# Performance work log

Measured on AMD Instinct MI355X. Metric: run time of the kernel, lower is better.

## Reference

```python
import jax, jax.numpy as jnp
import numpy as np
import itertools

# The repo's eset_ops_4_to_4 builds 69 permutation-equivariant basis ops on a
# rank-4 set tensor x[n, d, i, j, k, l]. We reconstruct the 69-dim basis as all
# order-preserving subset matchings (A, B) with A = kept input index slots,
# B = output slots receiving them (|A| = |B| = s, s = 1..4): sum x over the
# complement of A, then broadcast the reduced tensor into output positions B.
# Count: sum_{s=1..4} C(4,s)^2 = 16 + 36 + 16 + 1 = 69 (Vandermonde C(8,4)=70
# minus the s=0 global-sum term).

def _basis_pairs():
    pairs = []
    for s in range(1, 5):
        for A in itertools.combinations(range(4), s):
            for B in itertools.combinations(range(4), s):
                pairs.append((A, B))
    return pairs  # len == 69

_PAIRS = _basis_pairs()


def _forward(x, coefs, bias):
    # x: (n, d, N, N, N, N); coefs: (d, s_out, 69); bias: (1, s_out, 1,1,1,1)
    out_shape = (x.shape[0], coefs.shape[1]) + x.shape[2:]
    out = jnp.zeros(out_shape, x.dtype)
    for idx, (A, B) in enumerate(_PAIRS):
        sum_axes = tuple(2 + i for i in range(4) if i not in A)
        red = x.sum(axis=sum_axes) if sum_axes else x  # (n, d, N^|A|)
        # mix channels on the SMALL reduced tensor (op and channel mix commute)
        term = jnp.einsum('ds,nd...->ns...', coefs[:, :, idx], red)
        # place kept axes at output slots B (order-preserving), broadcast rest
        for p in range(4):
            if p not in B:
                term = jnp.expand_dims(term, axis=2 + p)
        out = out + term  # broadcasting add == broadcast then accumulate
    return out + bias


def setup_inputs() -> dict:
    key = jax.random.key(0)
    k1, k2 = jax.random.split(key)
    n, d, s_out, N, basis = 2, 8, 8, 32, 69
    x = jax.random.normal(k1, (n, d, N, N, N, N), dtype=jnp.float32)
    std = np.sqrt(2.0 / (d + s_out + basis)).astype(np.float32)
    coefs = std * jax.random.normal(k2, (d, s_out, basis), dtype=jnp.float32)
    bias = jnp.zeros((1, s_out, 1, 1, 1, 1), dtype=jnp.float32)
    return {'x': x, 'coefs': coefs, 'bias': bias}


def reference(x, coefs, bias):
    return _forward(x, coefs, bias)
```

## Files before the change

kernel.cpp:

```cpp
#include <hip/hip_runtime.h>


constexpr size_t R3SZ  = 524288;
constexpr size_t R2SZ  = 16384;
constexpr size_t R1SZ  = 512;
constexpr size_t R3OFF = 0;
constexpr size_t R2OFF = R3OFF + 4 * R3SZ;
constexpr size_t R1OFF = R2OFF + 6 * R2SZ;
constexpr size_t T2OFF = R1OFF + 4 * R1SZ;
constexpr size_t T1OFF = T2OFF + 6 * R2SZ;
constexpr size_t U3OFF = T1OFF + 4 * R1SZ;

__global__ __launch_bounds__(512) void k_red3(const float* __restrict__ x,
                                              float* __restrict__ ws) {
    __shared__ float4 cp[32][4][8];
    __shared__ float  b012[1024];
    __shared__ float4 a2[256];
    const int bid  = blockIdx.x;
    const int t    = threadIdx.x;
    const int half = t >> 8;
    const int tt   = t & 255;
    const int k    = tt >> 3;
    const int l4   = tt & 7;

    if (bid < 512) {
        const int i    = bid & 31;
        const int nd   = bid >> 5;
        const int w4   = (t >> 6) & 3;
        const int lane = t & 63;
        const float* xp = x + ((size_t)nd << 20) + ((size_t)i << 15) + k * 32 + l4 * 4;
        float4 acc = {0.f, 0.f, 0.f, 0.f};
        #pragma unroll
        for (int it = 0; it < 16; ++it) {
            const int j = it * 2 + half;
            float4 v = *(const float4*)(xp + j * 1024);
            acc.x += v.x; acc.y += v.y; acc.z += v.z; acc.w += v.w;
            float h = v.x + v.y + v.z + v.w;
            h += __shfl_xor(h, 1); h += __shfl_xor(h, 2); h += __shfl_xor(h, 4);
            if (l4 == 0) b012[j * 32 + k] = h;
            v.x += __shfl_xor(v.x, 8);  v.y += __shfl_xor(v.y, 8);
            v.z += __shfl_xor(v.z, 8);  v.w += __shfl_xor(v.w, 8);
            v.x += __shfl_xor(v.x, 16); v.y += __shfl_xor(v.y, 16);
            v.z += __shfl_xor(v.z, 16); v.w += __shfl_xor(v.w, 16);
            v.x += __shfl_xor(v.x, 32); v.y += __shfl_xor(v.y, 32);
            v.z += __shfl_xor(v.z, 32); v.w += __shfl_xor(v.w, 32);
            if (lane < 8) cp[j][w4][lane] = v;
        }
        if (half == 1) a2[tt] = acc;
        __syncthreads();
        const size_t base = ((size_t)nd << 15) + ((size_t)i << 10);
        *(float2*)(ws + R3OFF + base + 2 * t) = *(const float2*)(b012 + 2 * t);
        if (half == 0) {
            const int j = tt >> 3, lj = tt & 7;
            float4 s0 = cp[j][0][lj], s1 = cp[j][1][lj];
            float4 s2 = cp[j][2][lj], s3 = cp[j][3][lj];
            float4 s;
            s.x = s0.x + s1.x + s2.x + s3.x;
            s.y = s0.y + s1.y + s2.y + s3.y;
            s.z = s0.z + s1.z + s2.z + s3.z;
            s.w = s0.w + s1.w + s2.w + s3.w;
            *(float4*)(ws + R3OFF + R3SZ + base + j * 32 + lj * 4) = s;
            float4 b = a2[tt];
            a2[tt] = s;
            acc.x += b.x; acc.y += b.y; acc.z += b.z; acc.w += b.w;
            *(float4*)(ws + R3OFF + 2 * R3SZ + base + k * 32 + l4 * 4) = acc;
        }
        __syncthreads();
        const size_t r2b = (size_t)nd * 1024 + (size_t)i * 32;
        if (t < 32) {
            float s = 0.f;
            #pragma unroll
            for (int kk = 0; kk < 32; ++kk) s += b012[t * 32 + ((kk + t) & 31)];
            ws[R2OFF + 0 * R2SZ + r2b + t] = s;
        } else if (t < 64) {
            const int kc = t - 32;
            float s = 0.f;
            #pragma unroll
            for (int j = 0; j < 32; ++j) s += b012[j * 32 + kc];
            ws[R2OFF + 1 * R2SZ + r2b + kc] = s;
        } else if (t < 96) {
            const int l = t - 64;
            const float* af = (const float*)a2;
            float s = 0.f;
            #pragma unroll
            for (int j = 0; j < 32; ++j) s += af[j * 32 + l];
            ws[R2OFF + 2 * R2SZ + r2b + l] = s;
        }
    } else {
        const int bb = bid - 512;
        const int j  = bb & 31;
        const int nd = bb >> 5;
        const float* xp = x + ((size_t)nd << 20) + (size_t)j * 1024 + (size_t)tt * 4;
        float4 acc = {0.f, 0.f, 0.f, 0.f};
        #pragma unroll
        for (int it = 0; it < 16; ++it) {
            const int i = it * 2 + half;
            float4 v = *(const float4*)(xp + ((size_t)i << 15));
            acc.x += v.x; acc.y += v.y; acc.z += v.z; acc.w += v.w;
        }
        if (half == 1) a2[tt] = acc;
        __syncthreads();
        const size_t r2b = (size_t)nd * 1024 + (size_t)j * 32;
        if (half == 0) {
            float4 b = a2[tt];
            acc.x += b.x; acc.y += b.y; acc.z += b.z; acc.w += b.w;
            *(float4*)(ws + R3OFF + 3 * R3SZ + ((size_t)nd << 15)
                       + ((size_t)j << 10) + tt * 4) = acc;
            float h = acc.x + acc.y + acc.z + acc.w;
            h += __shfl_xor(h, 1); h += __shfl_xor(h, 2); h += __shfl_xor(h, 4);
            if ((t & 7) == 0) ws[R2OFF + 3 * R2SZ + r2b + k] = h;
            float4 c2 = acc;
            c2.x += __shfl_xor(c2.x, 8);  c2.y += __shfl_xor(c2.y, 8);
            c2.z += __shfl_xor(c2.z, 8);  c2.w += __shfl_xor(c2.w, 8);
            c2.x += __shfl_xor(c2.x, 16); c2.y += __shfl_xor(c2.y, 16);
            c2.z += __shfl_xor(c2.z, 16); c2.w += __shfl_xor(c2.w, 16);
            c2.x += __shfl_xor(c2.x, 32); c2.y += __shfl_xor(c2.y, 32);
            c2.z += __shfl_xor(c2.z, 32); c2.w += __shfl_xor(c2.w, 32);
            if ((t & 63) < 8) cp[0][t >> 6][t & 63] = c2;
        }
        __syncthreads();
        if (t < 8) {
            float4 s0 = cp[0][0][t], s1 = cp[0][1][t];
            float4 s2 = cp[0][2][t], s3 = cp[0][3][t];
            float4 s;
            s.x = s0.x + s1.x + s2.x + s3.x;
            s.y = s0.y + s1.y + s2.y + s3.y;
            s.z = s0.z + s1.z + s2.z + s3.z;
            s.w = s0.w + s1.w + s2.w + s3.w;
            *(float4*)(ws + R2OFF + 4 * R2SZ + r2b + t * 4) = s;
        }
    }
}

__global__ __launch_bounds__(256) void k_mixT(const float* __restrict__ coefs,
                                              float* __restrict__ ws) {
    __shared__ float cs[4416];
    __shared__ float s23[256];
    __shared__ float r1[1024];
    const int tt = threadIdx.x;
    for (int idx = tt; idx < 4416; idx += 256) cs[idx] = coefs[idx];
    const int b = blockIdx.x;
    if (b < 64) {
        const int n  = b >> 5;
        const int ch = b & 31;
        {
            const int d  = tt >> 5, q0 = tt & 31;
            const float* r023p = ws + R3OFF + 2 * R3SZ
                                 + ((size_t)(n * 8 + d) << 15) + ch * 32 + q0;
            float s = 0.f;
            #pragma unroll
            for (int i = 0; i < 32; ++i) s += r023p[i * 1024];
            s23[d * 32 + q0] = s;
        }
        __syncthreads();
        const int so = tt >> 5, pql = tt & 31;
        const int pq = ch * 32 + pql;
        float r2v[5][8];
        #pragma unroll
        for (int a2 = 0; a2 < 5; ++a2)
            #pragma unroll
            for (int d = 0; d < 8; ++d)
                r2v[a2][d] = ws[R2OFF + (size_t)a2 * R2SZ + (size_t)(n * 8 + d) * 1024 + pq];
        #pragma unroll
        for (int b2 = 0; b2 < 6; ++b2) {
            float s = 0.f;
            #pragma unroll
            for (int d = 0; d < 8; ++d) {
                const int cb = (d * 8 + so) * 69 + 16 + b2;
                #pragma unroll
                for (int a2 = 0; a2 < 5; ++a2) s += cs[cb + a2 * 6] * r2v[a2][d];
                s += cs[cb + 30] * s23[d * 32 + pql];
            }
            ws[T2OFF + (size_t)b2 * R2SZ + (size_t)(n * 8 + so) * 1024 + pq] = s;
        }
    } else {
        const int n = b - 64;
        {
            const int a1 = tt >> 6;
            const int dd = (tt >> 3) & 7;
            const int p0 = (tt & 7) * 4;
            const int src = (a1 == 0) ? 0 : ((a1 == 3) ? 4 : 3);
            const float* r2a = ws + R2OFF + (size_t)src * R2SZ + (size_t)(n * 8 + dd) * 1024;
            #pragma unroll
            for (int pp = 0; pp < 4; ++pp) {
                const int p = p0 + pp;
                float s = 0.f;
                if (a1 <= 1) { for (int q = 0; q < 32; ++q) s += r2a[p * 32 + q]; }
                else         { for (int q = 0; q < 32; ++q) s += r2a[q * 32 + p]; }
                r1[(a1 * 8 + dd) * 32 + p] = s;
            }
        }
        __syncthreads();
        const int so = tt >> 5, p = tt & 31;
        #pragma unroll
        for (int b1 = 0; b1 < 4; ++b1) {
            float s = 0.f;
            #pragma unroll
            for (int a1 = 0; a1 < 4; ++a1)
                #pragma unroll
                for (int d = 0; d < 8; ++d)
                    s += cs[(d * 8 + so) * 69 + a1 * 4 + b1] * r1[(a1 * 8 + d) * 32 + p];
            ws[T1OFF + (size_t)b1 * R1SZ + (size_t)(n * 8 + so) * 32 + p] = s;
        }
    }
}

__global__ __launch_bounds__(256) void k_mix3(const float* __restrict__ coefs,
                                              const float* __restrict__ bias,
                                              float* __restrict__ ws) {
    __shared__ float cs[4416];
    for (int idx = threadIdx.x; idx < 4416; idx += 256) cs[idx] = coefs[idx];
    __syncthreads();
    const int blk = blockIdx.x;
    const int cb  = blk & 127;
    const int sop = (blk >> 7) & 3;
    const int n   = blk >> 9;
    const int c   = cb * 256 + threadIdx.x;
    const int p1 = c >> 10, p2 = (c >> 5) & 31, p3 = c & 31;
    float v[4][8];
    #pragma unroll
    for (int a = 0; a < 4; ++a)
        #pragma unroll
        for (int d = 0; d < 8; ++d)
            v[a][d] = ws[R3OFF + (size_t)a * R3SZ + (size_t)(n * 8 + d) * 32768 + c];
    const float* T2 = ws + T2OFF;
    const float* T1 = ws + T1OFF;
    #pragma unroll
    for (int b = 0; b < 4; ++b) {
        #pragma unroll
        for (int so2 = 0; so2 < 2; ++so2) {
            const int so = sop * 2 + so2;
            float s = 0.f;
            #pragma unroll
            for (int a = 0; a < 4; ++a)
                #pragma unroll
                for (int d = 0; d < 8; ++d)
                    s += cs[(d * 8 + so) * 69 + 52 + a * 4 + b] * v[a][d];
            const size_t nso = (size_t)(n * 8 + so);
            if (b == 0) {
                s += T2[0 * R2SZ + nso * 1024 + p1 * 32 + p2];
                s += T2[1 * R2SZ + nso * 1024 + p1 * 32 + p3];
                s += T2[3 * R2SZ + nso * 1024 + p2 * 32 + p3];
                s += T1[0 * R1SZ + nso * 32 + p1];
                s += T1[1 * R1SZ + nso * 32 + p2];
                s += T1[2 * R1SZ + nso * 32 + p3];
                s += bias[so];
            } else if (b == 1) {
                s += T2[2 * R2SZ + nso * 1024 + p1 * 32 + p3];
                s += T2[4 * R2SZ + nso * 1024 + p2 * 32 + p3];
                s += T1[3 * R1SZ + nso * 32 + p3];
            } else if (b == 2) {
                s += T2[5 * R2SZ + nso * 1024 + p2 * 32 + p3];
            }
            ws[U3OFF + (size_t)b * R3SZ + nso * 32768 + c] = s;
        }
    }
}

__global__ __launch_bounds__(256) void k_final(const float* __restrict__ x,
                                               const float* __restrict__ coefs,
                                               const float* __restrict__ ws,
                                               float* __restrict__ out) {
    __shared__ float c68[64];
    if (threadIdx.x < 64) c68[threadIdx.x] = coefs[threadIdx.x * 69 + 68];
    __syncthreads();
    const int b = blockIdx.x;
    const int j = b & 31;
    const int i = (b >> 5) & 31;
    const int n = b >> 10;
    const int t = threadIdx.x;
    const int k = t >> 3, lq = t & 7;

    float4 xv[8];
    const float* xb = x + ((size_t)n << 23) + ((size_t)i << 15) + j * 1024 + k * 32 + lq * 4;
    #pragma unroll
    for (int d = 0; d < 8; ++d) xv[d] = *(const float4*)(xb + ((size_t)d << 20));

    const float* U = ws + U3OFF;
    const size_t c012 = (size_t)i * 1024 + j * 32 + k;
    const size_t c013 = (size_t)i * 1024 + j * 32 + lq * 4;
    const size_t c023 = (size_t)i * 1024 + k * 32 + lq * 4;
    const size_t c123 = (size_t)j * 1024 + k * 32 + lq * 4;

    #pragma unroll
    for (int so = 0; so < 8; ++so) {
        const size_t nso = (size_t)(n * 8 + so) << 15;
        const float  u0 = U[0 * R3SZ + nso + c012];
        const float4 u1 = *(const float4*)(U + 1 * R3SZ + nso + c013);
        const float4 u2 = *(const float4*)(U + 2 * R3SZ + nso + c023);
        const float4 u3 = *(const float4*)(U + 3 * R3SZ + nso + c123);
        float4 acc;
        acc.x = u0 + u1.x + u2.x + u3.x;
        acc.y = u0 + u1.y + u2.y + u3.y;
        acc.z = u0 + u1.z + u2.z + u3.z;
        acc.w = u0 + u1.w + u2.w + u3.w;
        #pragma unroll
        for (int d = 0; d < 8; ++d) {
            const float w = c68[d * 8 + so];
            acc.x += w * xv[d].x; acc.y += w * xv[d].y;
            acc.z += w * xv[d].z; acc.w += w * xv[d].w;
        }
        *(float4*)(out + ((size_t)(n * 8 + so) << 20) + ((size_t)i << 15)
                   + j * 1024 + k * 32 + lq * 4) = acc;
    }
}

extern "C" void kernel_launch(void* const* d_in, const int* in_sizes, int n_in,
                              void* d_out, int out_size, void* d_ws, size_t ws_size,
                              hipStream_t stream) {
    const float* x     = (const float*)d_in[0];
    const float* coefs = (const float*)d_in[1];
    const float* bias  = (const float*)d_in[2];
    float* out = (float*)d_out;
    float* ws  = (float*)d_ws;

    hipLaunchKernelGGL(k_red3, dim3(1024), dim3(512), 0, stream, x, ws);
    hipLaunchKernelGGL(k_mixT, dim3(66),   dim3(256), 0, stream, coefs, ws);
    hipLaunchKernelGGL(k_mix3, dim3(1024), dim3(256), 0, stream, coefs, bias, ws);
    hipLaunchKernelGGL(k_final, dim3(2048), dim3(256), 0, stream, x, coefs, ws, out);
}
```

Measured before the change: 171.2 us.

## Merge mixT and mix3 into one kernel with atomic ticket and flag sync

Fuses the small k_mixT kernel and the k_mix3 kernel into a single launch. Blocks take a role from an atomic ticket counter: the first 66 compute the T2/T1 partial terms and raise a release flag, and the rest preload their rank-3 inputs and then spin until the flag reaches 66 before consuming T2/T1. This removes one kernel launch and the serialization gap between them. It also remaps the block index in k_final so consecutive blocks spread across the n/i/j space, likely for better memory-channel or cache distribution. Counters are reset inside k_red3, and the spin-wait adds a risk of stalls if producer blocks are scheduled late.

Result: slower. 233.5 us (+36.3%).

```diff
diff --git a/kernel.cpp b/kernel.cpp
--- a/kernel.cpp
+++ b/kernel.cpp
@@ -22,6 +22,11 @@
     const int tt   = t & 255;
     const int k    = tt >> 3;
     const int l4   = tt & 7;
+
+    if (bid == 0 && t == 0) {
+        ((int*)(ws + R1OFF))[0]  = 0;
+        ((int*)(ws + R1OFF))[64] = 0;
+    }
 
     if (bid < 512) {
         const int i    = bid & 31;
@@ -132,127 +137,144 @@
     }
 }
 
-__global__ __launch_bounds__(256) void k_mixT(const float* __restrict__ coefs,
-                                              float* __restrict__ ws) {
+__global__ __launch_bounds__(256) void k_mid(const float* __restrict__ coefs,
+                                             const float* __restrict__ bias,
+                                             float* __restrict__ ws) {
     __shared__ float cs[4416];
     __shared__ float s23[256];
     __shared__ float r1[1024];
+    __shared__ int   tk;
     const int tt = threadIdx.x;
     for (int idx = tt; idx < 4416; idx += 256) cs[idx] = coefs[idx];
-    const int b = blockIdx.x;
-    if (b < 64) {
-        const int n  = b >> 5;
-        const int ch = b & 31;
-        {
-            const int d  = tt >> 5, q0 = tt & 31;
-            const float* r023p = ws + R3OFF + 2 * R3SZ
-                                 + ((size_t)(n * 8 + d) << 15) + ch * 32 + q0;
-            float s = 0.f;
-            #pragma unroll
-            for (int i = 0; i < 32; ++i) s += r023p[i * 1024];
-            s23[d * 32 + q0] = s;
-        }
-        __syncthreads();
-        const int so = tt >> 5, pql = tt & 31;
-        const int pq = ch * 32 + pql;
-        float r2v[5][8];
-        #pragma unroll
-        for (int a2 = 0; a2 < 5; ++a2)
+    int* const ctr  = (int*)(ws + R1OFF);
+    int* const flag = ctr + 64;
+    if (tt == 0)
+        tk = __hip_atomic_fetch_add(ctr, 1, __ATOMIC_RELAXED, __HIP_MEMORY_SCOPE_AGENT);
+    __syncthreads();
+    const int role = tk;
+
+    if (role < 66) {
+        if (role < 64) {
+            const int n  = role >> 5;
+            const int ch = role & 31;
+            {
+                const int d  = tt >> 5, q0 = tt & 31;
+                const float* r023p = ws + R3OFF + 2 * R3SZ
+                                     + ((size_t)(n * 8 + d) << 15) + ch * 32 + q0;
+                float s = 0.f;
+                #pragma unroll
+                for (int i = 0; i < 32; ++i) s += r023p[i * 1024];
+                s23[d * 32 + q0] = s;
+            }
+            __syncthreads();
+            const int so = tt >> 5, pql = tt & 31;
+            const int pq = ch * 32 + pql;
+            float r2v[5][8];
+            #pragma unroll
+            for (int a2 = 0; a2 < 5; ++a2)
+                #pragma unroll
+                for (int d = 0; d < 8; ++d)
+                    r2v[a2][d] = ws[R2OFF + (size_t)a2 * R2SZ
+                                    + (size_t)(n * 8 + d) * 1024 + pq];
+            #pragma unroll
+            for (int b2 = 0; b2 < 6; ++b2) {
+                float s = 0.f;
+                #pragma unroll
+                for (int d = 0; d < 8; ++d) {
+                    const int cb = (d * 8 + so) * 69 + 16 + b2;
+                    #pragma unroll
+                    for (int a2 = 0; a2 < 5; ++a2) s += cs[cb + a2 * 6] * r2v[a2][d];
+                    s += cs[cb + 30] * s23[d * 32 + pql];
+                }
+                ws[T2OFF + (size_t)b2 * R2SZ + (size_t)(n * 8 + so) * 1024 + pq] = s;
+            }
+        } else {
+            const int n = role - 64;
+            {
+                const int a1 = tt >> 6;
+                const int dd = (tt >> 3) & 7;
+                const int p0 = (tt & 7) * 4;
+                const int src = (a1 == 0) ? 0 : ((a1 == 3) ? 4 : 3);
+                const float* r2a = ws + R2OFF + (size_t)src * R2SZ
+                                   + (size_t)(n * 8 + dd) * 1024;
+                #pragma unroll
+                for (int pp = 0; pp < 4; ++pp) {
+                    const int p = p0 + pp;
+                    float s = 0.f;
+                    if (a1 <= 1) { for (int q = 0; q < 32; ++q) s += r2a[p * 32 + q]; }
+                    else         { for (int q = 0; q < 32; ++q) s += r2a[q * 32 + p]; }
+                    r1[(a1 * 8 + dd) * 32 + p] = s;
+                }
+            }
+            __syncthreads();
+            const int so = tt >> 5, p = tt & 31;
+            #pragma unroll
+            for (int b1 = 0; b1 < 4; ++b1) {
+                float s = 0.f;
+                #pragma unroll
+                for (int a1 = 0; a1 < 4; ++a1)
+                    #pragma unroll
+                    for (int d = 0; d < 8; ++d)
+                        s += cs[(d * 8 + so) * 69 + a1 * 4 + b1]
+                             * r1[(a1 * 8 + d) * 32 + p];
+                ws[T1OFF + (size_t)b1 * R1SZ + (size_t)(n * 8 + so) * 32 + p] = s;
+            }
+        }
+        __threadfence();
+        __syncthreads();
+        if (tt == 0)
+            __hip_atomic_fetch_add(flag, 1, __ATOMIC_RELEASE, __HIP_MEMORY_SCOPE_AGENT);
+    } else {
+        const int blk = role - 66;
+        const int cb  = blk & 127;
+        const int sop = (blk >> 7) & 3;
+        const int n   = blk >> 9;
+        const int c   = cb * 256 + tt;
+        const int p1 = c >> 10, p2 = (c >> 5) & 31, p3 = c & 31;
+        float v[4][8];
+        #pragma unroll
+        for (int a = 0; a < 4; ++a)
             #pragma unroll
             for (int d = 0; d < 8; ++d)
-                r2v[a2][d] = ws[R2OFF + (size_t)a2 * R2SZ + (size_t)(n * 8 + d) * 1024 + pq];
-        #pragma unroll
-        for (int b2 = 0; b2 < 6; ++b2) {
-            float s = 0.f;
-            #pragma unroll
-            for (int d = 0; d < 8; ++d) {
-                const int cb = (d * 8 + so) * 69 + 16 + b2;
-                #pragma unroll
-                for (int a2 = 0; a2 < 5; ++a2) s += cs[cb + a2 * 6] * r2v[a2][d];
-                s += cs[cb + 30] * s23[d * 32 + pql];
-            }
-            ws[T2OFF + (size_t)b2 * R2SZ + (size_t)(n * 8 + so) * 1024 + pq] = s;
-        }
-    } else {
-        const int n = b - 64;
-        {
-            const int a1 = tt >> 6;
-            const int dd = (tt >> 3) & 7;
-            const int p0 = (tt & 7) * 4;
-            const int src = (a1 == 0) ? 0 : ((a1 == 3) ? 4 : 3);
-            const float* r2a = ws + R2OFF + (size_t)src * R2SZ + (size_t)(n * 8 + dd) * 1024;
-            #pragma unroll
-            for (int pp = 0; pp < 4; ++pp) {
-                const int p = p0 + pp;
+                v[a][d] = ws[R3OFF + (size_t)a * R3SZ
+                             + (size_t)(n * 8 + d) * 32768 + c];
+        if (tt == 0) {
+            while (__hip_atomic_load(flag, __ATOMIC_ACQUIRE,
+                                     __HIP_MEMORY_SCOPE_AGENT) < 66)
+                __builtin_amdgcn_s_sleep(8);
+        }
+        __syncthreads();
+        const float* T2 = ws + T2OFF;
+        const float* T1 = ws + T1OFF;
+        #pragma unroll
+        for (int b = 0; b < 4; ++b) {
+            #pragma unroll
+            for (int so2 = 0; so2 < 2; ++so2) {
+                const int so = sop * 2 + so2;
                 float s = 0.f;
-                if (a1 <= 1) { for (int q = 0; q < 32; ++q) s += r2a[p * 32 + q]; }
-                else         { for (int q = 0; q < 32; ++q) s += r2a[q * 32 + p]; }
-                r1[(a1 * 8 + dd) * 32 + p] = s;
-            }
-        }
-        __syncthreads();
-        const int so = tt >> 5, p = tt & 31;
-        #pragma unroll
-        for (int b1 = 0; b1 < 4; ++b1) {
-            float s = 0.f;
-            #pragma unroll
-            for (int a1 = 0; a1 < 4; ++a1)
-                #pragma unroll
-                for (int d = 0; d < 8; ++d)
-                    s += cs[(d * 8 + so) * 69 + a1 * 4 + b1] * r1[(a1 * 8 + d) * 32 + p];
-            ws[T1OFF + (size_t)b1 * R1SZ + (size_t)(n * 8 + so) * 32 + p] = s;
-        }
-    }
-}
-
-__global__ __launch_bounds__(256) void k_mix3(const float* __restrict__ coefs,
-                                              const float* __restrict__ bias,
-                                              float* __restrict__ ws) {
-    __shared__ float cs[4416];
-    for (int idx = threadIdx.x; idx < 4416; idx += 256) cs[idx] = coefs[idx];
-    __syncthreads();
-    const int blk = blockIdx.x;
-    const int cb  = blk & 127;
-    const int sop = (blk >> 7) & 3;
-    const int n   = blk >> 9;
-    const int c   = cb * 256 + threadIdx.x;
-    const int p1 = c >> 10, p2 = (c >> 5) & 31, p3 = c & 31;
-    float v[4][8];
-    #pragma unroll
-    for (int a = 0; a < 4; ++a)
-        #pragma unroll
-        for (int d = 0; d < 8; ++d)
-            v[a][d] = ws[R3OFF + (size_t)a * R3SZ + (size_t)(n * 8 + d) * 32768 + c];
-    const float* T2 = ws + T2OFF;
-    const float* T1 = ws + T1OFF;
-    #pragma unroll
-    for (int b = 0; b < 4; ++b) {
-        #pragma unroll
-        for (int so2 = 0; so2 < 2; ++so2) {
-            const int so = sop * 2 + so2;
-            float s = 0.f;
-            #pragma unroll
-            for (int a = 0; a < 4; ++a)
-                #pragma unroll
-                for (int d = 0; d < 8; ++d)
-                    s += cs[(d * 8 + so) * 69 + 52 + a * 4 + b] * v[a][d];
-            const size_t nso = (size_t)(n * 8 + so);
-            if (b == 0) {
-                s += T2[0 * R2SZ + nso * 1024 + p1 * 32 + p2];
-                s += T2[1 * R2SZ + nso * 1024 + p1 * 32 + p3];
-                s += T2[3 * R2SZ + nso * 1024 + p2 * 32 + p3];
-                s += T1[0 * R1SZ + nso * 32 + p1];
-                s += T1[1 * R1SZ + nso * 32 + p2];
-                s += T1[2 * R1SZ + nso * 32 + p3];
-                s += bias[so];
-            } else if (b == 1) {
-                s += T2[2 * R2SZ + nso * 1024 + p1 * 32 + p3];
-                s += T2[4 * R2SZ + nso * 1024 + p2 * 32 + p3];
-                s += T1[3 * R1SZ + nso * 32 + p3];
-            } else if (b == 2) {
-                s += T2[5 * R2SZ + nso * 1024 + p2 * 32 + p3];
-            }
-            ws[U3OFF + (size_t)b * R3SZ + nso * 32768 + c] = s;
+                #pragma unroll
+                for (int a = 0; a < 4; ++a)
+                    #pragma unroll
+                    for (int d = 0; d < 8; ++d)
+                        s += cs[(d * 8 + so) * 69 + 52 + a * 4 + b] * v[a][d];
+                const size_t nso = (size_t)(n * 8 + so);
+                if (b == 0) {
+                    s += T2[0 * R2SZ + nso * 1024 + p1 * 32 + p2];
+                    s += T2[1 * R2SZ + nso * 1024 + p1 * 32 + p3];
+                    s += T2[3 * R2SZ + nso * 1024 + p2 * 32 + p3];
+                    s += T1[0 * R1SZ + nso * 32 + p1];
+                    s += T1[1 * R1SZ + nso * 32 + p2];
+                    s += T1[2 * R1SZ + nso * 32 + p3];
+                    s += bias[so];
+                } else if (b == 1) {
+                    s += T2[2 * R2SZ + nso * 1024 + p1 * 32 + p3];
+                    s += T2[4 * R2SZ + nso * 1024 + p2 * 32 + p3];
+                    s += T1[3 * R1SZ + nso * 32 + p3];
+                } else if (b == 2) {
+                    s += T2[5 * R2SZ + nso * 1024 + p2 * 32 + p3];
+                }
+                ws[U3OFF + (size_t)b * R3SZ + nso * 32768 + c] = s;
+            }
         }
     }
 }
@@ -264,7 +286,8 @@
     __shared__ float c68[64];
     if (threadIdx.x < 64) c68[threadIdx.x] = coefs[threadIdx.x * 69 + 68];
     __syncthreads();
-    const int b = blockIdx.x;
+    const int rb = blockIdx.x;
+    const int b  = ((rb & 7) << 8) | (rb >> 3);
     const int j = b & 31;
     const int i = (b >> 5) & 31;
     const int n = b >> 10;
@@ -315,7 +338,6 @@
     float* ws  = (float*)d_ws;
 
     hipLaunchKernelGGL(k_red3, dim3(1024), dim3(512), 0, stream, x, ws);
-    hipLaunchKernelGGL(k_mixT, dim3(66),   dim3(256), 0, stream, coefs, ws);
-    hipLaunchKernelGGL(k_mix3, dim3(1024), dim3(256), 0, stream, coefs, bias, ws);
+    hipLaunchKernelGGL(k_mid,  dim3(1090), dim3(256), 0, stream, coefs, bias, ws);
     hipLaunchKernelGGL(k_final, dim3(2048), dim3(256), 0, stream, x, coefs, ws, out);
 }
```

## Fold small-tensor channel mixing into k_mix3 and drop k_mixT launch

Applied to the files above, without the earlier changes.

Removes the separate k_mixT kernel. The rank-2 and rank-1 reductions are now finished inside k_red3, using atomics and wave shuffles into slots zeroed by a memset beforehand. k_mix3 then recomputes the T2/T1 channel-mix contributions per element on the fly instead of reading precomputed tables. This saves a launch and a serialized low-parallelism kernel, but adds redundant per-thread mixing arithmetic and gathered loads in k_mix3, atomic contention in k_red3, and an extra memset. k_final's block index is also swizzled to change the order in which memory is accessed.

Measured after the change: 213.6 us. +24.7%, slower.

```diff
diff --git a/kernel.cpp b/kernel.cpp
--- a/kernel.cpp
+++ b/kernel.cpp
@@ -7,9 +7,7 @@
 constexpr size_t R3OFF = 0;
 constexpr size_t R2OFF = R3OFF + 4 * R3SZ;
 constexpr size_t R1OFF = R2OFF + 6 * R2SZ;
-constexpr size_t T2OFF = R1OFF + 4 * R1SZ;
-constexpr size_t T1OFF = T2OFF + 6 * R2SZ;
-constexpr size_t U3OFF = T1OFF + 4 * R1SZ;
+constexpr size_t U3OFF = R1OFF + 4 * R1SZ;
 
 __global__ __launch_bounds__(512) void k_red3(const float* __restrict__ x,
                                               float* __restrict__ ws) {
@@ -64,6 +62,9 @@
             a2[tt] = s;
             acc.x += b.x; acc.y += b.y; acc.z += b.z; acc.w += b.w;
             *(float4*)(ws + R3OFF + 2 * R3SZ + base + k * 32 + l4 * 4) = acc;
+            float* r23 = ws + R2OFF + 5 * R2SZ + (size_t)nd * 1024 + k * 32 + l4 * 4;
+            atomicAdd(r23 + 0, acc.x); atomicAdd(r23 + 1, acc.y);
+            atomicAdd(r23 + 2, acc.z); atomicAdd(r23 + 3, acc.w);
         }
         __syncthreads();
         const size_t r2b = (size_t)nd * 1024 + (size_t)i * 32;
@@ -72,12 +73,17 @@
             #pragma unroll
             for (int kk = 0; kk < 32; ++kk) s += b012[t * 32 + ((kk + t) & 31)];
             ws[R2OFF + 0 * R2SZ + r2b + t] = s;
+            float r = s;
+            r += __shfl_xor(r, 1);  r += __shfl_xor(r, 2);  r += __shfl_xor(r, 4);
+            r += __shfl_xor(r, 8);  r += __shfl_xor(r, 16);
+            if (t == 0) ws[R1OFF + 0 * R1SZ + (size_t)nd * 32 + i] = r;
         } else if (t < 64) {
             const int kc = t - 32;
             float s = 0.f;
             #pragma unroll
             for (int j = 0; j < 32; ++j) s += b012[j * 32 + kc];
             ws[R2OFF + 1 * R2SZ + r2b + kc] = s;
+            atomicAdd(ws + R1OFF + 2 * R1SZ + (size_t)nd * 32 + kc, s);
         } else if (t < 96) {
             const int l = t - 64;
             const float* af = (const float*)a2;
@@ -85,6 +91,7 @@
             #pragma unroll
             for (int j = 0; j < 32; ++j) s += af[j * 32 + l];
             ws[R2OFF + 2 * R2SZ + r2b + l] = s;
+            atomicAdd(ws + R1OFF + 3 * R1SZ + (size_t)nd * 32 + l, s);
         }
     } else {
         const int bb = bid - 512;
@@ -108,7 +115,10 @@
                        + ((size_t)j << 10) + tt * 4) = acc;
             float h = acc.x + acc.y + acc.z + acc.w;
             h += __shfl_xor(h, 1); h += __shfl_xor(h, 2); h += __shfl_xor(h, 4);
-            if ((t & 7) == 0) ws[R2OFF + 3 * R2SZ + r2b + k] = h;
+            if ((t & 7) == 0) {
+                ws[R2OFF + 3 * R2SZ + r2b + k] = h;
+                b012[k] = h;
+            }
             float4 c2 = acc;
             c2.x += __shfl_xor(c2.x, 8);  c2.y += __shfl_xor(c2.y, 8);
             c2.z += __shfl_xor(c2.z, 8);  c2.w += __shfl_xor(c2.w, 8);
@@ -129,78 +139,11 @@
             s.w = s0.w + s1.w + s2.w + s3.w;
             *(float4*)(ws + R2OFF + 4 * R2SZ + r2b + t * 4) = s;
         }
-    }
-}
-
-__global__ __launch_bounds__(256) void k_mixT(const float* __restrict__ coefs,
-                                              float* __restrict__ ws) {
-    __shared__ float cs[4416];
-    __shared__ float s23[256];
-    __shared__ float r1[1024];
-    const int tt = threadIdx.x;
-    for (int idx = tt; idx < 4416; idx += 256) cs[idx] = coefs[idx];
-    const int b = blockIdx.x;
-    if (b < 64) {
-        const int n  = b >> 5;
-        const int ch = b & 31;
-        {
-            const int d  = tt >> 5, q0 = tt & 31;
-            const float* r023p = ws + R3OFF + 2 * R3SZ
-                                 + ((size_t)(n * 8 + d) << 15) + ch * 32 + q0;
-            float s = 0.f;
-            #pragma unroll
-            for (int i = 0; i < 32; ++i) s += r023p[i * 1024];
-            s23[d * 32 + q0] = s;
-        }
-        __syncthreads();
-        const int so = tt >> 5, pql = tt & 31;
-        const int pq = ch * 32 + pql;
-        float r2v[5][8];
-        #pragma unroll
-        for (int a2 = 0; a2 < 5; ++a2)
-            #pragma unroll
-            for (int d = 0; d < 8; ++d)
-                r2v[a2][d] = ws[R2OFF + (size_t)a2 * R2SZ + (size_t)(n * 8 + d) * 1024 + pq];
-        #pragma unroll
-        for (int b2 = 0; b2 < 6; ++b2) {
-            float s = 0.f;
-            #pragma unroll
-            for (int d = 0; d < 8; ++d) {
-                const int cb = (d * 8 + so) * 69 + 16 + b2;
-                #pragma unroll
-                for (int a2 = 0; a2 < 5; ++a2) s += cs[cb + a2 * 6] * r2v[a2][d];
-                s += cs[cb + 30] * s23[d * 32 + pql];
-            }
-            ws[T2OFF + (size_t)b2 * R2SZ + (size_t)(n * 8 + so) * 1024 + pq] = s;
-        }
-    } else {
-        const int n = b - 64;
-        {
-            const int a1 = tt >> 6;
-            const int dd = (tt >> 3) & 7;
-            const int p0 = (tt & 7) * 4;
-            const int src = (a1 == 0) ? 0 : ((a1 == 3) ? 4 : 3);
-            const float* r2a = ws + R2OFF + (size_t)src * R2SZ + (size_t)(n * 8 + dd) * 1024;
-            #pragma unroll
-            for (int pp = 0; pp < 4; ++pp) {
-                const int p = p0 + pp;
-                float s = 0.f;
-                if (a1 <= 1) { for (int q = 0; q < 32; ++q) s += r2a[p * 32 + q]; }
-                else         { for (int q = 0; q < 32; ++q) s += r2a[q * 32 + p]; }
-                r1[(a1 * 8 + dd) * 32 + p] = s;
-            }
-        }
-        __syncthreads();
-        const int so = tt >> 5, p = tt & 31;
-        #pragma unroll
-        for (int b1 = 0; b1 < 4; ++b1) {
-            float s = 0.f;
-            #pragma unroll
-            for (int a1 = 0; a1 < 4; ++a1)
-                #pragma unroll
-                for (int d = 0; d < 8; ++d)
-                    s += cs[(d * 8 + so) * 69 + a1 * 4 + b1] * r1[(a1 * 8 + d) * 32 + p];
-            ws[T1OFF + (size_t)b1 * R1SZ + (size_t)(n * 8 + so) * 32 + p] = s;
+        if (t < 32) {
+            float r = b012[t];
+            r += __shfl_xor(r, 1);  r += __shfl_xor(r, 2);  r += __shfl_xor(r, 4);
+            r += __shfl_xor(r, 8);  r += __shfl_xor(r, 16);
+            if (t == 0) ws[R1OFF + 1 * R1SZ + (size_t)nd * 32 + j] = r;
         }
     }
 }
@@ -217,14 +160,53 @@
     const int n   = blk >> 9;
     const int c   = cb * 256 + threadIdx.x;
     const int p1 = c >> 10, p2 = (c >> 5) & 31, p3 = c & 31;
+    const int idxA = p1 * 32 + p2, idxB = p1 * 32 + p3, idxC = p2 * 32 + p3;
+
+    float t2f[2][6] = {};
+    #pragma unroll
+    for (int a2 = 0; a2 < 6; ++a2) {
+        #pragma unroll
+        for (int d = 0; d < 8; ++d) {
+            const float* base = ws + R2OFF + (size_t)a2 * R2SZ
+                                + (size_t)(n * 8 + d) * 1024;
+            const float vA = base[idxA], vB = base[idxB], vC = base[idxC];
+            #pragma unroll
+            for (int so2 = 0; so2 < 2; ++so2) {
+                const int cc = (d * 8 + sop * 2 + so2) * 69 + 16 + a2 * 6;
+                t2f[so2][0] += cs[cc + 0] * vA;
+                t2f[so2][1] += cs[cc + 1] * vB;
+                t2f[so2][2] += cs[cc + 3] * vC;
+                t2f[so2][3] += cs[cc + 2] * vB;
+                t2f[so2][4] += cs[cc + 4] * vC;
+                t2f[so2][5] += cs[cc + 5] * vC;
+            }
+        }
+    }
+    float t1f[2][4] = {};
+    #pragma unroll
+    for (int a1 = 0; a1 < 4; ++a1) {
+        #pragma unroll
+        for (int d = 0; d < 8; ++d) {
+            const float* base = ws + R1OFF + (size_t)a1 * R1SZ
+                                + (size_t)(n * 8 + d) * 32;
+            const float v1 = base[p1], v2 = base[p2], v3 = base[p3];
+            #pragma unroll
+            for (int so2 = 0; so2 < 2; ++so2) {
+                const int cc = (d * 8 + sop * 2 + so2) * 69 + a1 * 4;
+                t1f[so2][0] += cs[cc + 0] * v1;
+                t1f[so2][1] += cs[cc + 1] * v2;
+                t1f[so2][2] += cs[cc + 2] * v3;
+                t1f[so2][3] += cs[cc + 3] * v3;
+            }
+        }
+    }
+
     float v[4][8];
     #pragma unroll
     for (int a = 0; a < 4; ++a)
         #pragma unroll
         for (int d = 0; d < 8; ++d)
             v[a][d] = ws[R3OFF + (size_t)a * R3SZ + (size_t)(n * 8 + d) * 32768 + c];
-    const float* T2 = ws + T2OFF;
-    const float* T1 = ws + T1OFF;
     #pragma unroll
     for (int b = 0; b < 4; ++b) {
         #pragma unroll
@@ -236,23 +218,16 @@
                 #pragma unroll
                 for (int d = 0; d < 8; ++d)
                     s += cs[(d * 8 + so) * 69 + 52 + a * 4 + b] * v[a][d];
-            const size_t nso = (size_t)(n * 8 + so);
             if (b == 0) {
-                s += T2[0 * R2SZ + nso * 1024 + p1 * 32 + p2];
-                s += T2[1 * R2SZ + nso * 1024 + p1 * 32 + p3];
-                s += T2[3 * R2SZ + nso * 1024 + p2 * 32 + p3];
-                s += T1[0 * R1SZ + nso * 32 + p1];
-                s += T1[1 * R1SZ + nso * 32 + p2];
-                s += T1[2 * R1SZ + nso * 32 + p3];
+                s += t2f[so2][0] + t2f[so2][1] + t2f[so2][2];
+                s += t1f[so2][0] + t1f[so2][1] + t1f[so2][2];
                 s += bias[so];
             } else if (b == 1) {
-                s += T2[2 * R2SZ + nso * 1024 + p1 * 32 + p3];
-                s += T2[4 * R2SZ + nso * 1024 + p2 * 32 + p3];
-                s += T1[3 * R1SZ + nso * 32 + p3];
+                s += t2f[so2][3] + t2f[so2][4] + t1f[so2][3];
             } else if (b == 2) {
-                s += T2[5 * R2SZ + nso * 1024 + p2 * 32 + p3];
-            }
-            ws[U3OFF + (size_t)b * R3SZ + nso * 32768 + c] = s;
+                s += t2f[so2][5];
+            }
+            ws[U3OFF + (size_t)b * R3SZ + (size_t)(n * 8 + so) * 32768 + c] = s;
         }
     }
 }
@@ -264,7 +239,8 @@
     __shared__ float c68[64];
     if (threadIdx.x < 64) c68[threadIdx.x] = coefs[threadIdx.x * 69 + 68];
     __syncthreads();
-    const int b = blockIdx.x;
+    const int rb = blockIdx.x;
+    const int b  = ((rb & 7) << 8) | (rb >> 3);
     const int j = b & 31;
     const int i = (b >> 5) & 31;
     const int n = b >> 10;
@@ -314,8 +290,9 @@
     float* out = (float*)d_out;
     float* ws  = (float*)d_ws;
 
-    hipLaunchKernelGGL(k_red3, dim3(1024), dim3(512), 0, stream, x, ws);
-    hipLaunchKernelGGL(k_mixT, dim3(66),   dim3(256), 0, stream, coefs, ws);
-    hipLaunchKernelGGL(k_mix3, dim3(1024), dim3(256), 0, stream, coefs, bias, ws);
+    hipMemsetAsync((void*)(ws + R2OFF + 5 * R2SZ), 0,
+                   (R2SZ + 4 * R1SZ) * sizeof(float), stream);
+    hipLaunchKernelGGL(k_red3,  dim3(1024), dim3(512), 0, stream, x, ws);
+    hipLaunchKernelGGL(k_mix3,  dim3(1024), dim3(256), 0, stream, coefs, bias, ws);
     hipLaunchKernelGGL(k_final, dim3(2048), dim3(256), 0, stream, x, coefs, ws, out);
 }
```
